# Optimization experiments

Measured on AMD Instinct MI355X. Metric: run time of the kernel, lower is better.

## Reference

```python
import jax, jax.numpy as jnp
import numpy as np

N_NODES = 200000
N_EDGES = 6400000
N_GRAPHS = 128


def setup_inputs() -> dict:
    key = jax.random.key(0)
    k1, k2, k3, k4, k5, k6, k7 = jax.random.split(key, 7)
    x = jax.random.normal(k1, (N_NODES, 1), dtype=jnp.float32)
    edge_index = jax.random.randint(k2, (2, N_EDGES), 0, N_NODES, dtype=jnp.int64)
    batch = jnp.sort(jax.random.randint(k3, (N_NODES,), 0, N_GRAPHS, dtype=jnp.int64))
    # GCNConv parameters (glorot-ish scale)
    W1 = jax.random.normal(k4, (1, 32), dtype=jnp.float32) * (1.0 / np.sqrt(1 + 32))
    b1 = jnp.zeros((32,), dtype=jnp.float32)
    W2 = jax.random.normal(k5, (32, 8), dtype=jnp.float32) * (1.0 / np.sqrt(32 + 8))
    b2 = jnp.zeros((8,), dtype=jnp.float32)
    return {"x": x, "edge_index": edge_index, "batch": batch,
            "W1": W1, "b1": b1, "W2": W2, "b2": b2}


def _gcn_conv(x, src, dst, W, b):
    # x: [N, din] -> [N, dout]; PyG GCNConv: symmetric-normalized A+I aggregation
    h = x @ W                                            # [N, dout]
    deg = jax.ops.segment_sum(jnp.ones_like(dst, h.dtype), dst, num_segments=N_NODES)
    dinv = jnp.where(deg > 0, jax.lax.rsqrt(deg), 0.0)    # [N]
    norm = dinv[src] * dinv[dst]                          # [E+N]
    msg = h[src] * norm[:, None]                          # gather + scale
    out = jax.ops.segment_sum(msg, dst, num_segments=N_NODES)
    return out + b


def reference(x, edge_index, batch, W1, b1, W2, b2):
    loop = jnp.arange(N_NODES, dtype=edge_index.dtype)
    src = jnp.concatenate([edge_index[0], loop])          # add self-loops
    dst = jnp.concatenate([edge_index[1], loop])
    h = _gcn_conv(x, src, dst, W1, b1)
    h = _gcn_conv(h, src, dst, W2, b2)
    # global mean pool over graphs
    sums = jax.ops.segment_sum(h, batch, num_segments=N_GRAPHS)
    cnts = jax.ops.segment_sum(jnp.ones((N_NODES,), h.dtype), batch, num_segments=N_GRAPHS)
    pooled = sums / jnp.maximum(cnts, 1.0)[:, None]       # [G, 8]
    return jax.nn.log_softmax(pooled, axis=1)
```

## Files before the change

### kernel.cpp

```cpp
#include <hip/hip_runtime.h>
#include <math.h>

#define N_NODES 200000
#define N_EDGES 6400000
#define N_GRAPHS 128
#define NI4     (N_EDGES / 4)

#define NBKC  128
#define CBSZ  1568
#define CAP   51712
#define CHK   8000
#define CHK4  (CHK / 4)
#define PBLK  (N_EDGES / CHK)
#define NSUB8 8

static __device__ __forceinline__ unsigned bc_of(unsigned n) { return n / (unsigned)CBSZ; }

__global__ void __launch_bounds__(512)
kP1_partition(const int* __restrict__ src, const int* __restrict__ dst,
              unsigned* __restrict__ gcur, unsigned* __restrict__ binned) {
    __shared__ unsigned cnt[NBKC];
    __shared__ unsigned ofs[NBKC];
    __shared__ unsigned cur[NBKC];
    __shared__ unsigned gofs[NBKC];
    __shared__ unsigned stage[CHK];
    const int tid = threadIdx.x;
    if (tid < NBKC) cnt[tid] = 0;
    __syncthreads();

    const int base4 = blockIdx.x * CHK4;
    const int4* s4 = (const int4*)src;
    const int4* d4 = (const int4*)dst;
    int4 sv[4], dv[4];
    bool ok[4];
    #pragma unroll
    for (int k = 0; k < 4; ++k) {
        int e = tid + k * 512;
        ok[k] = (e < CHK4);
        int ec = ok[k] ? e : 0;
        sv[k] = s4[base4 + ec];
        dv[k] = d4[base4 + ec];
    }
    #pragma unroll
    for (int k = 0; k < 4; ++k) {
        if (ok[k]) {
            atomicAdd(&cnt[bc_of((unsigned)dv[k].x)], 1u);
            atomicAdd(&cnt[bc_of((unsigned)dv[k].y)], 1u);
            atomicAdd(&cnt[bc_of((unsigned)dv[k].z)], 1u);
            atomicAdd(&cnt[bc_of((unsigned)dv[k].w)], 1u);
        }
    }
    __syncthreads();
    if (tid < 64) {
        unsigned v0 = cnt[tid];
        unsigned s0 = v0;
        for (int off = 1; off < 64; off <<= 1) {
            unsigned u = __shfl_up(s0, off);
            if (tid >= off) s0 += u;
        }
        unsigned tot0 = __shfl(s0, 63);
        unsigned v1 = cnt[64 + tid];
        unsigned s1 = v1;
        for (int off = 1; off < 64; off <<= 1) {
            unsigned u = __shfl_up(s1, off);
            if (tid >= off) s1 += u;
        }
        ofs[tid] = s0 - v0;
        ofs[64 + tid] = tot0 + s1 - v1;
    }
    __syncthreads();
    if (tid < NBKC) {
        gofs[tid] = atomicAdd(&gcur[tid], cnt[tid]);
        cur[tid] = ofs[tid];
    }
    __syncthreads();
    #pragma unroll
    for (int k = 0; k < 4; ++k) {
        if (ok[k]) {
            unsigned p;
            unsigned b0 = bc_of((unsigned)dv[k].x), l0 = (unsigned)dv[k].x - b0 * CBSZ;
            unsigned b1 = bc_of((unsigned)dv[k].y), l1 = (unsigned)dv[k].y - b1 * CBSZ;
            unsigned b2 = bc_of((unsigned)dv[k].z), l2 = (unsigned)dv[k].z - b2 * CBSZ;
            unsigned b3 = bc_of((unsigned)dv[k].w), l3 = (unsigned)dv[k].w - b3 * CBSZ;
            p = atomicAdd(&cur[b0], 1u); stage[p] = ((unsigned)sv[k].x << 11) | l0;
            p = atomicAdd(&cur[b1], 1u); stage[p] = ((unsigned)sv[k].y << 11) | l1;
            p = atomicAdd(&cur[b2], 1u); stage[p] = ((unsigned)sv[k].z << 11) | l2;
            p = atomicAdd(&cur[b3], 1u); stage[p] = ((unsigned)sv[k].w << 11) | l3;
        }
    }
    __syncthreads();
    const int wave = tid >> 6, lane = tid & 63;
    for (int b = wave; b < NBKC; b += 8) {
        unsigned o = ofs[b];
        unsigned end = (b < NBKC - 1) ? ofs[b + 1] : (unsigned)CHK;
        unsigned c = end - o;
        unsigned gb = gofs[b];
        if (gb >= (unsigned)CAP) continue;
        unsigned avail = (unsigned)CAP - gb;
        if (c > avail) c = avail;
        unsigned gbase = (unsigned)b * CAP + gb;
        for (unsigned i = lane; i < c; i += 64)
            binned[gbase + i] = stage[o + i];
    }
}

static __device__ __forceinline__ void sub_range(unsigned cnt, int sub,
                                                 unsigned& s_, unsigned& e_) {
    unsigned per4 = (((cnt + NSUB8 - 1) / NSUB8) + 3u) & ~3u;
    unsigned s = (unsigned)sub * per4;
    if (s > cnt) s = cnt;
    unsigned e = s + per4;
    if (e > cnt) e = cnt;
    s_ = s; e_ = e;
}

__global__ void __launch_bounds__(512)
kB_deg(const unsigned* __restrict__ binned, const unsigned* __restrict__ gcur,
       unsigned* __restrict__ part) {
    __shared__ unsigned bins[CBSZ];
    const int tid = threadIdx.x;
    for (int l = tid; l < CBSZ; l += 512) bins[l] = 0;
    __syncthreads();
    const int bkt = blockIdx.x >> 3, sub = blockIdx.x & 7;
    unsigned cnt = gcur[bkt];
    if (cnt > (unsigned)CAP) cnt = CAP;
    unsigned s, e;
    sub_range(cnt, sub, s, e);
    const unsigned base = (unsigned)bkt * CAP;
    const unsigned a0 = base + s, a1 = base + e;
    const uint4* b4 = (const uint4*)binned;
    for (unsigned q = (a0 >> 2) + tid; q < (a1 >> 2); q += 512) {
        uint4 v = b4[q];
        atomicAdd(&bins[v.x & 2047u], 1u);
        atomicAdd(&bins[v.y & 2047u], 1u);
        atomicAdd(&bins[v.z & 2047u], 1u);
        atomicAdd(&bins[v.w & 2047u], 1u);
    }
    unsigned t0 = a1 & ~3u;
    if (t0 >= a0 && tid < (int)(a1 - t0)) atomicAdd(&bins[binned[t0 + tid] & 2047u], 1u);
    __syncthreads();
    unsigned* dstp = part + (size_t)blockIdx.x * CBSZ;
    for (int l = tid; l < CBSZ; l += 512) dstp[l] = bins[l];
}

__global__ void __launch_bounds__(512)
kRedB(const unsigned* __restrict__ part, const float* __restrict__ x,
      float2* __restrict__ pairBD) {
    int n = blockIdx.x * 512 + threadIdx.x;
    if (n >= N_NODES) return;
    unsigned b = bc_of((unsigned)n);
    unsigned l = (unsigned)n - b * CBSZ;
    const unsigned* p = part + (size_t)(b * NSUB8) * CBSZ + l;
    unsigned d = 0;
    #pragma unroll
    for (int j = 0; j < NSUB8; ++j) d += p[(size_t)j * CBSZ];
    float di = rsqrtf((float)d + 1.0f);
    pairBD[n] = make_float2(x[n] * di, di);
}

__global__ void __launch_bounds__(512)
kC_pass1(const unsigned* __restrict__ binned, const unsigned* __restrict__ gcur,
         const float2* __restrict__ pairBD, const int* __restrict__ batch,
         float* __restrict__ partF, float* __restrict__ gacc) {
    __shared__ float binsT[CBSZ];
    __shared__ float binsS[CBSZ];
    __shared__ float gl[N_GRAPHS];
    const int tid = threadIdx.x;
    for (int l = tid; l < CBSZ; l += 512) { binsT[l] = 0.0f; binsS[l] = 0.0f; }
    if (tid < N_GRAPHS) gl[tid] = 0.0f;
    __syncthreads();
    const int bkt = blockIdx.x >> 3, sub = blockIdx.x & 7;
    unsigned cnt = gcur[bkt];
    if (cnt > (unsigned)CAP) cnt = CAP;
    unsigned s, e;
    sub_range(cnt, sub, s, e);
    const unsigned base = (unsigned)bkt * CAP;
    const unsigned a0 = base + s, a1 = base + e;
    const uint4* b4 = (const uint4*)binned;
    for (unsigned q = (a0 >> 2) + tid; q < (a1 >> 2); q += 512) {
        uint4 v = b4[q];
        float2 p0 = pairBD[v.x >> 11];
        float2 p1 = pairBD[v.y >> 11];
        float2 p2 = pairBD[v.z >> 11];
        float2 p3 = pairBD[v.w >> 11];
        atomicAdd(&binsT[v.x & 2047u], p0.x); atomicAdd(&binsS[v.x & 2047u], p0.y);
        atomicAdd(&binsT[v.y & 2047u], p1.x); atomicAdd(&binsS[v.y & 2047u], p1.y);
        atomicAdd(&binsT[v.z & 2047u], p2.x); atomicAdd(&binsS[v.z & 2047u], p2.y);
        atomicAdd(&binsT[v.w & 2047u], p3.x); atomicAdd(&binsS[v.w & 2047u], p3.y);
    }
    unsigned t0 = a1 & ~3u;
    if (t0 >= a0 && tid < (int)(a1 - t0)) {
        unsigned v = binned[t0 + tid];
        float2 p = pairBD[v >> 11];
        atomicAdd(&binsT[v & 2047u], p.x);
        atomicAdd(&binsS[v & 2047u], p.y);
    }
    __syncthreads();
    float* dT = partF + (size_t)blockIdx.x * CBSZ;
    for (int l = tid; l < CBSZ; l += 512) {
        dT[l] = binsT[l];
        int node = bkt * CBSZ + l;
        if (node < N_NODES) {
            float v = pairBD[node].y * binsS[l];
            if (v != 0.0f) atomicAdd(&gl[batch[node]], v);
        }
    }
    __syncthreads();
    if (tid < N_GRAPHS) {
        float v = gl[tid];
        if (v != 0.0f) atomicAdd(&gacc[N_GRAPHS + tid], v);
    }
}

__global__ void __launch_bounds__(512)
kRedC(const float* __restrict__ partF, const float2* __restrict__ pairBD,
      const int* __restrict__ batch, float* __restrict__ adi, float* __restrict__ gacc) {
    int n = blockIdx.x * 512 + threadIdx.x;
    bool valid = (n < N_NODES);
    float c1 = 0.0f, c0 = 0.0f, cc = 0.0f;
    int g = 0;
    if (valid) {
        unsigned b = bc_of((unsigned)n);
        unsigned l = (unsigned)n - b * CBSZ;
        const float* p = partF + (size_t)(b * NSUB8) * CBSZ + l;
        float t1 = 0.0f;
        #pragma unroll
        for (int j = 0; j < NSUB8; ++j) t1 += p[(size_t)j * CBSZ];
        float2 pb = pairBD[n];
        float xd = pb.x, di = pb.y;
        g = batch[n];
        float a = di * (t1 + xd);
        float ad = a * di;
        adi[n] = ad;
        c1 = di * ad;
        c0 = di * di;
        cc = 1.0f;
    }
    int tid = threadIdx.x;
    int g0 = __shfl(g, 0);
    bool uni = __all(!valid || (g == g0));
    if (uni) {
        for (int off = 32; off; off >>= 1) {
            c1 += __shfl_down(c1, off);
            c0 += __shfl_down(c0, off);
            cc += __shfl_down(cc, off);
        }
        if ((tid & 63) == 0) {
            atomicAdd(&gacc[g0], c1);
            atomicAdd(&gacc[N_GRAPHS + g0], c0);
            atomicAdd(&gacc[2 * N_GRAPHS + g0], cc);
        }
    } else if (valid) {
        atomicAdd(&gacc[g], c1);
        atomicAdd(&gacc[N_GRAPHS + g], c0);
        atomicAdd(&gacc[2 * N_GRAPHS + g], 1.0f);
    }
}

__global__ void __launch_bounds__(512)
kD2_pass2(const unsigned* __restrict__ binned, const unsigned* __restrict__ gcur,
          const float* __restrict__ adi, const float2* __restrict__ pairBD,
          const int* __restrict__ batch, float* __restrict__ gacc) {
    __shared__ float bins[CBSZ];
    __shared__ float gl[N_GRAPHS];
    const int tid = threadIdx.x;
    for (int l = tid; l < CBSZ; l += 512) bins[l] = 0.0f;
    if (tid < N_GRAPHS) gl[tid] = 0.0f;
    __syncthreads();
    const int bkt = blockIdx.x >> 3, sub = blockIdx.x & 7;
    unsigned cnt = gcur[bkt];
    if (cnt > (unsigned)CAP) cnt = CAP;
    unsigned s, e;
    sub_range(cnt, sub, s, e);
    const unsigned base = (unsigned)bkt * CAP;
    const unsigned a0 = base + s, a1 = base + e;
    const uint4* b4 = (const uint4*)binned;
    for (unsigned q = (a0 >> 2) + tid; q < (a1 >> 2); q += 512) {
        uint4 v = b4[q];
        float g0 = adi[v.x >> 11], g1 = adi[v.y >> 11], g2 = adi[v.z >> 11], g3 = adi[v.w >> 11];
        atomicAdd(&bins[v.x & 2047u], g0);
        atomicAdd(&bins[v.y & 2047u], g1);
        atomicAdd(&bins[v.z & 2047u], g2);
        atomicAdd(&bins[v.w & 2047u], g3);
    }
    unsigned t0 = a1 & ~3u;
    if (t0 >= a0 && tid < (int)(a1 - t0)) {
        unsigned v = binned[t0 + tid];
        atomicAdd(&bins[v & 2047u], adi[v >> 11]);
    }
    __syncthreads();
    for (int l = tid; l < CBSZ; l += 512) {
        int node = bkt * CBSZ + l;
        if (node < N_NODES) {
            float v = pairBD[node].y * bins[l];
            if (v != 0.0f) atomicAdd(&gl[batch[node]], v);
        }
    }
    __syncthreads();
    if (tid < N_GRAPHS) {
        float v = gl[tid];
        if (v != 0.0f) atomicAdd(&gacc[tid], v);
    }
}

__global__ void k_final(const float* __restrict__ gacc,
                        const float* __restrict__ W1, const float* __restrict__ b1,
                        const float* __restrict__ W2, const float* __restrict__ b2,
                        float* __restrict__ out) {
    int g = threadIdx.x;
    if (g >= N_GRAPHS) return;
    float GS1 = gacc[g];
    float GS0 = gacc[N_GRAPHS + g];
    float cnt = gacc[2 * N_GRAPHS + g];
    float denom = fmaxf(cnt, 1.0f);
    float p[8];
    for (int k = 0; k < 8; ++k) {
        float u = 0.0f, v = 0.0f;
        for (int c = 0; c < 32; ++c) {
            u += W1[c] * W2[c * 8 + k];
            v += b1[c] * W2[c * 8 + k];
        }
        p[k] = (u * GS1 + v * GS0 + cnt * b2[k]) / denom;
    }
    float m = p[0];
    for (int k = 1; k < 8; ++k) m = fmaxf(m, p[k]);
    float s = 0.0f;
    for (int k = 0; k < 8; ++k) s += expf(p[k] - m);
    float l = logf(s);
    for (int k = 0; k < 8; ++k) out[g * 8 + k] = p[k] - m - l;
}

__global__ void k_deg(const int* __restrict__ dst, float* __restrict__ deg) {
    const int4* d4 = (const int4*)dst;
    for (int e = blockIdx.x * blockDim.x + threadIdx.x; e < NI4; e += gridDim.x * blockDim.x) {
        int4 d = d4[e];
        atomicAdd(&deg[d.x], 1.0f); atomicAdd(&deg[d.y], 1.0f);
        atomicAdd(&deg[d.z], 1.0f); atomicAdd(&deg[d.w], 1.0f);
    }
}
__global__ void k_dinv(const float* __restrict__ x, float* __restrict__ deg_dinv,
                       float* __restrict__ xd) {
    int i = blockIdx.x * blockDim.x + threadIdx.x;
    if (i < N_NODES) {
        float dinv = rsqrtf(deg_dinv[i] + 1.0f);
        deg_dinv[i] = dinv;
        xd[i] = x[i] * dinv;
    }
}
__global__ void k_pass1(const int* __restrict__ src, const int* __restrict__ dst,
                        const float* __restrict__ xd, float* __restrict__ t) {
    const int4* s4 = (const int4*)src;
    const int4* d4 = (const int4*)dst;
    for (int e = blockIdx.x * blockDim.x + threadIdx.x; e < NI4; e += gridDim.x * blockDim.x) {
        int4 s = s4[e]; int4 d = d4[e];
        atomicAdd(&t[d.x], xd[s.x]); atomicAdd(&t[d.y], xd[s.y]);
        atomicAdd(&t[d.z], xd[s.z]); atomicAdd(&t[d.w], xd[s.w]);
    }
}
__global__ void k_agg1(const float* __restrict__ dinv, const float* __restrict__ xd,
                       float* __restrict__ t, float2* __restrict__ pair) {
    int i = blockIdx.x * blockDim.x + threadIdx.x;
    if (i < N_NODES) {
        float di = dinv[i];
        float a = di * (t[i] + xd[i]);
        t[i] = a;
        pair[i] = make_float2(a * di, di);
    }
}
__global__ void k_pass2(const int* __restrict__ src, const int* __restrict__ dst,
                        const float2* __restrict__ pair,
                        float* __restrict__ s1, float* __restrict__ s0) {
    const int4* s4 = (const int4*)src;
    const int4* d4 = (const int4*)dst;
    for (int e = blockIdx.x * blockDim.x + threadIdx.x; e < NI4; e += gridDim.x * blockDim.x) {
        int4 s = s4[e]; int4 d = d4[e];
        float2 p0 = pair[s.x], p1 = pair[s.y], p2 = pair[s.z], p3 = pair[s.w];
        atomicAdd(&s1[d.x], p0.x); atomicAdd(&s0[d.x], p0.y);
        atomicAdd(&s1[d.y], p1.x); atomicAdd(&s0[d.y], p1.y);
        atomicAdd(&s1[d.z], p2.x); atomicAdd(&s0[d.z], p2.y);
        atomicAdd(&s1[d.w], p3.x); atomicAdd(&s0[d.w], p3.y);
    }
}
__global__ void k_node2(const float* __restrict__ dinv, const float* __restrict__ agg1,
                        const float* __restrict__ s1, const float* __restrict__ s0,
                        const int* __restrict__ batch, float* __restrict__ gacc) {
    int i = blockIdx.x * blockDim.x + threadIdx.x;
    float s1f = 0.0f, s0f = 0.0f; int g = 0;
    bool valid = (i < N_NODES);
    if (valid) {
        float di = dinv[i];
        s1f = di * (s1[i] + agg1[i] * di);
        s0f = di * (s0[i] + di);
        g = batch[i];
    }
    int g0 = __shfl(g, 0);
    bool uni = __all(valid && (g == g0));
    if (uni) {
        for (int off = 32; off; off >>= 1) {
            s1f += __shfl_down(s1f, off);
            s0f += __shfl_down(s0f, off);
        }
        if ((threadIdx.x & 63) == 0) {
            atomicAdd(&gacc[g0], s1f);
            atomicAdd(&gacc[N_GRAPHS + g0], s0f);
            atomicAdd(&gacc[2 * N_GRAPHS + g0], 64.0f);
        }
    } else if (valid) {
        atomicAdd(&gacc[g], s1f);
        atomicAdd(&gacc[N_GRAPHS + g], s0f);
        atomicAdd(&gacc[2 * N_GRAPHS + g], 1.0f);
    }
}


extern "C" void kernel_launch(void* const* d_in, const int* in_sizes, int n_in,
                              void* d_out, int out_size, void* d_ws, size_t ws_size,
                              hipStream_t stream) {
    const float* x     = (const float*)d_in[0];
    const int*   edge  = (const int*)d_in[1];
    const int*   batch = (const int*)d_in[2];
    const float* W1    = (const float*)d_in[3];
    const float* b1    = (const float*)d_in[4];
    const float* W2    = (const float*)d_in[5];
    const float* b2    = (const float*)d_in[6];
    float* out = (float*)d_out;

    const int* src = edge;
    const int* dst = edge + N_EDGES;

    const size_t o_binned = 0;
    const size_t o_gcur   = o_binned + (size_t)NBKC * CAP;
    const size_t o_part   = o_gcur + NBKC;
    const size_t o_pairBD = o_part + (size_t)NBKC * NSUB8 * CBSZ;
    const size_t o_adi    = o_pairBD + 2 * (size_t)N_NODES;
    const size_t o_gacc   = o_adi + N_NODES;
    const size_t need_u32 = o_gacc + 3 * N_GRAPHS;

    unsigned* ws_u = (unsigned*)d_ws;
    float*    ws_f = (float*)d_ws;

    if (ws_size >= need_u32 * 4) {
        unsigned* binned  = ws_u + o_binned;
        unsigned* gcur    = ws_u + o_gcur;
        unsigned* partU   = ws_u + o_part;
        float*    partF   = (float*)(ws_u + o_part);
        float2*   pairBD  = (float2*)(ws_f + o_pairBD);
        float*    adi     = ws_f + o_adi;
        float*    gacc    = ws_f + o_gacc;

        hipMemsetAsync(gcur, 0, NBKC * sizeof(unsigned), stream);
        hipMemsetAsync(gacc, 0, 3 * N_GRAPHS * sizeof(float), stream);

        kP1_partition<<<PBLK, 512, 0, stream>>>(src, dst, gcur, binned);
        kB_deg       <<<NBKC * NSUB8, 512, 0, stream>>>(binned, gcur, partU);
        kRedB        <<<(N_NODES + 511) / 512, 512, 0, stream>>>(partU, x, pairBD);
        kC_pass1     <<<NBKC * NSUB8, 512, 0, stream>>>(binned, gcur, pairBD, batch, partF, gacc);
        kRedC        <<<(N_NODES + 511) / 512, 512, 0, stream>>>(partF, pairBD, batch, adi, gacc);
        kD2_pass2    <<<NBKC * NSUB8, 512, 0, stream>>>(binned, gcur, adi, pairBD, batch, gacc);
        k_final      <<<1, 128, 0, stream>>>(gacc, W1, b1, W2, b2, out);
    } else {
        float* dinv = ws_f;
        float* t    = ws_f + 1 * N_NODES;
        float* s1   = ws_f + 2 * N_NODES;
        float* s0   = ws_f + 3 * N_NODES;
        float* xd   = ws_f + 4 * N_NODES;
        float2* pair = (float2*)(ws_f + 6 * N_NODES);
        float* gacc = ws_f + 8 * N_NODES;

        hipMemsetAsync(ws_f, 0, (size_t)4 * N_NODES * sizeof(float), stream);
        hipMemsetAsync(gacc, 0, (size_t)3 * N_GRAPHS * sizeof(float), stream);

        const int EB = 2048, ET = 256;
        const int NB = (N_NODES + 255) / 256, NT = 256;

        k_deg  <<<EB, ET, 0, stream>>>(dst, dinv);
        k_dinv <<<NB, NT, 0, stream>>>(x, dinv, xd);
        k_pass1<<<EB, ET, 0, stream>>>(src, dst, xd, t);
        k_agg1 <<<NB, NT, 0, stream>>>(dinv, xd, t, pair);
        k_pass2<<<EB, ET, 0, stream>>>(src, dst, pair, s1, s0);
        k_node2<<<NB, NT, 0, stream>>>(dinv, t, s1, s0, batch, gacc);
        k_final<<<1, 128, 0, stream>>>(gacc, W1, b1, W2, b2, out);
    }
}
```

Baseline: 221.2 us.

## Store gather pair as half2 and double-unroll edge loops in passes

```diff
diff --git a/kernel.cpp b/kernel.cpp
--- a/kernel.cpp
+++ b/kernel.cpp
@@ -1,4 +1,5 @@
 #include <hip/hip_runtime.h>
+#include <hip/hip_fp16.h>
 #include <math.h>
 
 #define N_NODES 200000
@@ -145,7 +146,7 @@
 
 __global__ void __launch_bounds__(512)
 kRedB(const unsigned* __restrict__ part, const float* __restrict__ x,
-      float2* __restrict__ pairBD) {
+      __half2* __restrict__ pairH, float* __restrict__ diF) {
     int n = blockIdx.x * 512 + threadIdx.x;
     if (n >= N_NODES) return;
     unsigned b = bc_of((unsigned)n);
@@ -155,12 +156,14 @@
     #pragma unroll
     for (int j = 0; j < NSUB8; ++j) d += p[(size_t)j * CBSZ];
     float di = rsqrtf((float)d + 1.0f);
-    pairBD[n] = make_float2(x[n] * di, di);
+    pairH[n] = __floats2half2_rn(x[n] * di, di);
+    diF[n] = di;
 }
 
 __global__ void __launch_bounds__(512)
 kC_pass1(const unsigned* __restrict__ binned, const unsigned* __restrict__ gcur,
-         const float2* __restrict__ pairBD, const int* __restrict__ batch,
+         const __half2* __restrict__ pairH, const float* __restrict__ diF,
+         const int* __restrict__ batch,
          float* __restrict__ partF, float* __restrict__ gacc) {
     __shared__ float binsT[CBSZ];
     __shared__ float binsS[CBSZ];
@@ -177,21 +180,34 @@
     const unsigned base = (unsigned)bkt * CAP;
     const unsigned a0 = base + s, a1 = base + e;
     const uint4* b4 = (const uint4*)binned;
-    for (unsigned q = (a0 >> 2) + tid; q < (a1 >> 2); q += 512) {
+    const unsigned qe = a1 >> 2;
+    for (unsigned q = (a0 >> 2) + tid; q < qe; q += 1024) {
         uint4 v = b4[q];
-        float2 p0 = pairBD[v.x >> 11];
-        float2 p1 = pairBD[v.y >> 11];
-        float2 p2 = pairBD[v.z >> 11];
-        float2 p3 = pairBD[v.w >> 11];
+        bool has2 = (q + 512u) < qe;
+        uint4 w = has2 ? b4[q + 512u] : v;
+        float2 p0 = __half22float2(pairH[v.x >> 11]);
+        float2 p1 = __half22float2(pairH[v.y >> 11]);
+        float2 p2 = __half22float2(pairH[v.z >> 11]);
+        float2 p3 = __half22float2(pairH[v.w >> 11]);
+        float2 r0 = __half22float2(pairH[w.x >> 11]);
+        float2 r1 = __half22float2(pairH[w.y >> 11]);
+        float2 r2 = __half22float2(pairH[w.z >> 11]);
+        float2 r3 = __half22float2(pairH[w.w >> 11]);
         atomicAdd(&binsT[v.x & 2047u], p0.x); atomicAdd(&binsS[v.x & 2047u], p0.y);
         atomicAdd(&binsT[v.y & 2047u], p1.x); atomicAdd(&binsS[v.y & 2047u], p1.y);
         atomicAdd(&binsT[v.z & 2047u], p2.x); atomicAdd(&binsS[v.z & 2047u], p2.y);
         atomicAdd(&binsT[v.w & 2047u], p3.x); atomicAdd(&binsS[v.w & 2047u], p3.y);
+        if (has2) {
+            atomicAdd(&binsT[w.x & 2047u], r0.x); atomicAdd(&binsS[w.x & 2047u], r0.y);
+            atomicAdd(&binsT[w.y & 2047u], r1.x); atomicAdd(&binsS[w.y & 2047u], r1.y);
+            atomicAdd(&binsT[w.z & 2047u], r2.x); atomicAdd(&binsS[w.z & 2047u], r2.y);
+            atomicAdd(&binsT[w.w & 2047u], r3.x); atomicAdd(&binsS[w.w & 2047u], r3.y);
+        }
     }
     unsigned t0 = a1 & ~3u;
     if (t0 >= a0 && tid < (int)(a1 - t0)) {
         unsigned v = binned[t0 + tid];
-        float2 p = pairBD[v >> 11];
+        float2 p = __half22float2(pairH[v >> 11]);
         atomicAdd(&binsT[v & 2047u], p.x);
         atomicAdd(&binsS[v & 2047u], p.y);
     }
@@ -201,7 +217,7 @@
         dT[l] = binsT[l];
         int node = bkt * CBSZ + l;
         if (node < N_NODES) {
-            float v = pairBD[node].y * binsS[l];
+            float v = diF[node] * binsS[l];
             if (v != 0.0f) atomicAdd(&gl[batch[node]], v);
         }
     }
@@ -213,8 +229,9 @@
 }
 
 __global__ void __launch_bounds__(512)
-kRedC(const float* __restrict__ partF, const float2* __restrict__ pairBD,
-      const int* __restrict__ batch, float* __restrict__ adi, float* __restrict__ gacc) {
+kRedC(const float* __restrict__ partF, const float* __restrict__ x,
+      const float* __restrict__ diF, const int* __restrict__ batch,
+      float* __restrict__ adi, float* __restrict__ gacc) {
     int n = blockIdx.x * 512 + threadIdx.x;
     bool valid = (n < N_NODES);
     float c1 = 0.0f, c0 = 0.0f, cc = 0.0f;
@@ -226,8 +243,8 @@
         float t1 = 0.0f;
         #pragma unroll
         for (int j = 0; j < NSUB8; ++j) t1 += p[(size_t)j * CBSZ];
-        float2 pb = pairBD[n];
-        float xd = pb.x, di = pb.y;
+        float di = diF[n];
+        float xd = x[n] * di;
         g = batch[n];
         float a = di * (t1 + xd);
         float ad = a * di;
@@ -259,7 +276,7 @@
 
 __global__ void __launch_bounds__(512)
 kD2_pass2(const unsigned* __restrict__ binned, const unsigned* __restrict__ gcur,
-          const float* __restrict__ adi, const float2* __restrict__ pairBD,
+          const float* __restrict__ adi, const float* __restrict__ diF,
           const int* __restrict__ batch, float* __restrict__ gacc) {
     __shared__ float bins[CBSZ];
     __shared__ float gl[N_GRAPHS];
@@ -275,13 +292,25 @@
     const unsigned base = (unsigned)bkt * CAP;
     const unsigned a0 = base + s, a1 = base + e;
     const uint4* b4 = (const uint4*)binned;
-    for (unsigned q = (a0 >> 2) + tid; q < (a1 >> 2); q += 512) {
+    const unsigned qe = a1 >> 2;
+    for (unsigned q = (a0 >> 2) + tid; q < qe; q += 1024) {
         uint4 v = b4[q];
-        float g0 = adi[v.x >> 11], g1 = adi[v.y >> 11], g2 = adi[v.z >> 11], g3 = adi[v.w >> 11];
+        bool has2 = (q + 512u) < qe;
+        uint4 w = has2 ? b4[q + 512u] : v;
+        float g0 = adi[v.x >> 11], g1 = adi[v.y >> 11];
+        float g2 = adi[v.z >> 11], g3 = adi[v.w >> 11];
+        float h0 = adi[w.x >> 11], h1 = adi[w.y >> 11];
+        float h2 = adi[w.z >> 11], h3 = adi[w.w >> 11];
         atomicAdd(&bins[v.x & 2047u], g0);
         atomicAdd(&bins[v.y & 2047u], g1);
         atomicAdd(&bins[v.z & 2047u], g2);
         atomicAdd(&bins[v.w & 2047u], g3);
+        if (has2) {
+            atomicAdd(&bins[w.x & 2047u], h0);
+            atomicAdd(&bins[w.y & 2047u], h1);
+            atomicAdd(&bins[w.z & 2047u], h2);
+            atomicAdd(&bins[w.w & 2047u], h3);
+        }
     }
     unsigned t0 = a1 & ~3u;
     if (t0 >= a0 && tid < (int)(a1 - t0)) {
@@ -292,7 +321,7 @@
     for (int l = tid; l < CBSZ; l += 512) {
         int node = bkt * CBSZ + l;
         if (node < N_NODES) {
-            float v = pairBD[node].y * bins[l];
+            float v = diF[node] * bins[l];
             if (v != 0.0f) atomicAdd(&gl[batch[node]], v);
         }
     }
@@ -431,8 +460,9 @@
     const size_t o_binned = 0;
     const size_t o_gcur   = o_binned + (size_t)NBKC * CAP;
     const size_t o_part   = o_gcur + NBKC;
-    const size_t o_pairBD = o_part + (size_t)NBKC * NSUB8 * CBSZ;
-    const size_t o_adi    = o_pairBD + 2 * (size_t)N_NODES;
+    const size_t o_pairH  = o_part + (size_t)NBKC * NSUB8 * CBSZ;
+    const size_t o_diF    = o_pairH + N_NODES;
+    const size_t o_adi    = o_diF + N_NODES;
     const size_t o_gacc   = o_adi + N_NODES;
     const size_t need_u32 = o_gacc + 3 * N_GRAPHS;
 
@@ -444,7 +474,8 @@
         unsigned* gcur    = ws_u + o_gcur;
         unsigned* partU   = ws_u + o_part;
         float*    partF   = (float*)(ws_u + o_part);
-        float2*   pairBD  = (float2*)(ws_f + o_pairBD);
+        __half2*  pairH   = (__half2*)(ws_u + o_pairH);
+        float*    diF     = ws_f + o_diF;
         float*    adi     = ws_f + o_adi;
         float*    gacc    = ws_f + o_gacc;
 
@@ -453,10 +484,10 @@
 
         kP1_partition<<<PBLK, 512, 0, stream>>>(src, dst, gcur, binned);
         kB_deg       <<<NBKC * NSUB8, 512, 0, stream>>>(binned, gcur, partU);
-        kRedB        <<<(N_NODES + 511) / 512, 512, 0, stream>>>(partU, x, pairBD);
-        kC_pass1     <<<NBKC * NSUB8, 512, 0, stream>>>(binned, gcur, pairBD, batch, partF, gacc);
-        kRedC        <<<(N_NODES + 511) / 512, 512, 0, stream>>>(partF, pairBD, batch, adi, gacc);
-        kD2_pass2    <<<NBKC * NSUB8, 512, 0, stream>>>(binned, gcur, adi, pairBD, batch, gacc);
+        kRedB        <<<(N_NODES + 511) / 512, 512, 0, stream>>>(partU, x, pairH, diF);
+        kC_pass1     <<<NBKC * NSUB8, 512, 0, stream>>>(binned, gcur, pairH, diF, batch, partF, gacc);
+        kRedC        <<<(N_NODES + 511) / 512, 512, 0, stream>>>(partF, x, diF, batch, adi, gacc);
+        kD2_pass2    <<<NBKC * NSUB8, 512, 0, stream>>>(binned, gcur, adi, diF, batch, gacc);
         k_final      <<<1, 128, 0, stream>>>(gacc, W1, b1, W2, b2, out);
     } else {
         float* dinv = ws_f;
```

Result: no change. 223.1 us (+0.9%).
